# Kernel tuning notes

Measured on AMD Instinct MI355X. Metric: run time of the kernel, lower is better.

Reference implementation:

```python
import jax, jax.numpy as jnp
import numpy as np

B, T_HIST, T_OUT, T_FC = 4096, 168, 48, 49
N_LABELS, F_CTL, F_FC, HID = 64, 16, 8, 32
EPS = 1e-7


def setup_inputs() -> dict:
    key = jax.random.key(0)
    ks = jax.random.split(key, 18)
    rn = lambda k, s, sc=1.0: jax.random.normal(k, s, jnp.float32) * sc
    return {
        "history": rn(ks[0], (B, T_HIST, N_LABELS)),
        "control": rn(ks[1], (B, T_OUT, F_CTL)),
        "forecasts": rn(ks[2], (B, T_FC, F_FC)),
        "h_mean": rn(ks[3], (N_LABELS,), 0.1),
        "h_var": jax.random.uniform(ks[4], (N_LABELS,), jnp.float32, 0.5, 1.5),
        "c_mean": rn(ks[5], (F_CTL,), 0.1),
        "c_var": jax.random.uniform(ks[6], (F_CTL,), jnp.float32, 0.5, 1.5),
        "f_mean": rn(ks[7], (), 0.1),
        "f_var": jax.random.uniform(ks[8], (), jnp.float32, 0.5, 1.5),
        "conv_w": rn(ks[9], (2, F_FC, 4), 0.2),   # kernel_size=2, Conv1D(4)
        "conv_b": rn(ks[10], (4,), 0.01),
        "lstm_k": rn(ks[11], (N_LABELS, 4 * HID), 0.1),
        "lstm_rk": rn(ks[12], (HID, 4 * HID), 0.1),
        "lstm_b": rn(ks[13], (4 * HID,), 0.01),
        "w1": rn(ks[14], (HID + F_CTL + 4, 64), 0.1),
        "b1": rn(ks[15], (64,), 0.01),
        "w2": rn(ks[16], (64, N_LABELS), 0.05),
        "b2": rn(ks[17], (N_LABELS,), 0.01),
    }


def _norm(x, m, v):
    # keras Normalization: (x - mean) / max(sqrt(var), eps)
    return (x - m) / jnp.maximum(jnp.sqrt(v), EPS)


def _lstm(x, h, c, k, rk, b):
    z = x @ k + h @ rk + b                      # [B, 4*HID], gate order i,f,g,o
    i, f, g, o = jnp.split(z, 4, axis=-1)
    c2 = jax.nn.sigmoid(f) * c + jax.nn.sigmoid(i) * jnp.tanh(g)
    h2 = jax.nn.sigmoid(o) * jnp.tanh(c2)
    return h2, c2


def _mlp(x1, x2, x3, w1, b1, w2, b2):
    x = jnp.concatenate([x1, x2, x3], axis=-1)  # [B, 52]
    return jax.nn.relu(x @ w1 + b1) @ w2 + b2


def reference(history, control, forecasts, h_mean, h_var, c_mean, c_var,
              f_mean, f_var, conv_w, conv_b, lstm_k, lstm_rk, lstm_b,
              w1, b1, w2, b2):
    latest = history[:, -1, :]                               # [B, N_LABELS]
    cn = _norm(control, c_mean, c_var)                       # [B, T_OUT, F_CTL]
    fn = _norm(forecasts, f_mean, f_var)                     # scalar norm
    # Conv1D(filters=4, kernel_size=2), valid padding -> [B, T_FC-1, 4]
    fc = fn[:, :-1] @ conv_w[0] + fn[:, 1:] @ conv_w[1] + conv_b

    # encoder LSTM over normalized history
    hn = _norm(history, h_mean, h_var)
    bsz = history.shape[0]
    init = (jnp.zeros((bsz, HID), hn.dtype), jnp.zeros((bsz, HID), hn.dtype))

    def enc_step(carry, x):
        h, c = carry
        return _lstm(x, h, c, lstm_k, lstm_rk, lstm_b), None

    (h, c), _ = jax.lax.scan(enc_step, init, jnp.swapaxes(hn, 0, 1))

    # pre-loop step (its prediction write is overwritten by loop i=0, but it
    # updates `latest` which feeds the loop)
    latest = latest + _mlp(h, cn[:, 0], fc[:, 0], w1, b1, w2, b2)

    t_out = control.shape[1]

    def dec_step(carry, inp):
        latest, h, c = carry
        ctl, fci = inp
        xn = _norm(latest, h_mean, h_var)
        h2, c2 = _lstm(xn, h, c, lstm_k, lstm_rk, lstm_b)
        latest2 = latest + _mlp(h2, ctl, fci, w1, b1, w2, b2)
        return (latest2, h2, c2), latest2

    xs = (jnp.swapaxes(cn, 0, 1), jnp.swapaxes(fc[:, :t_out], 0, 1))
    _, preds = jax.lax.scan(dec_step, (latest, h, c), xs)   # [T_OUT, B, N]
    return jnp.swapaxes(preds, 0, 1)                        # [B, T_OUT, N]
```

## Files before the change

kernel.cpp:

```cpp
#include <hip/hip_runtime.h>

#define EPSV 1e-7f

typedef __bf16 bf16x8 __attribute__((ext_vector_type(8)));
typedef float  f32x4  __attribute__((ext_vector_type(4)));
typedef unsigned int   u32x4 __attribute__((ext_vector_type(4)));
typedef unsigned short u16x8 __attribute__((ext_vector_type(8)));
typedef unsigned short u16x4 __attribute__((ext_vector_type(4)));

__device__ __forceinline__ unsigned short f2bf(float f) {
    unsigned int u = __float_as_uint(f);
    return (unsigned short)((u + 0x7FFFu + ((u >> 16) & 1u)) >> 16);
}
__device__ __forceinline__ float bf2f(unsigned short u) {
    return __uint_as_float(((unsigned int)u) << 16);
}
__device__ __forceinline__ void split2(float f, unsigned short& hi, unsigned short& lo) {
    hi = f2bf(f);
    lo = f2bf(f - bf2f(hi));
}
__device__ __forceinline__ void splitT(float f, unsigned short& hi, unsigned short& lo) {
    unsigned int u  = __float_as_uint(f);
    unsigned int hb = u & 0xFFFF0000u;
    float l = f - __uint_as_float(hb);
    hi = (unsigned short)(u >> 16);
    lo = (unsigned short)(__float_as_uint(l) >> 16);
}
__device__ __forceinline__ float sigf(float x) {
    return __builtin_amdgcn_rcpf(1.0f + __expf(-x));
}
__device__ __forceinline__ float tanhfast(float x) {
    float cx = fminf(fmaxf(x, -15.0f), 15.0f);
    float e = __expf(2.0f * cx);
    return (e - 1.0f) * __builtin_amdgcn_rcpf(e + 1.0f);
}
__device__ __forceinline__ float xor8(float v) {
    return __builtin_bit_cast(float, __builtin_amdgcn_update_dpp(
        0, __builtin_bit_cast(int, v), 0x128, 0xF, 0xF, true));
}

#define MFMA16(A, B, C) __builtin_amdgcn_mfma_f32_16x16x32_bf16(A, B, C, 0, 0, 0)
#define BC8(x) __builtin_bit_cast(bf16x8, x)

#define BARRIER() do {                                        \
    asm volatile("s_waitcnt lgkmcnt(0)" ::: "memory");        \
    __builtin_amdgcn_s_barrier();                             \
    __builtin_amdgcn_sched_barrier(0);                        \
} while (0)

#define HS2 72
#define MS  136
#define XS2 136
#define ZS3 20

__global__ __launch_bounds__(512) void tutina_kernel(
    const float* __restrict__ history, const float* __restrict__ control,
    const float* __restrict__ forecasts,
    const float* __restrict__ h_mean, const float* __restrict__ h_var,
    const float* __restrict__ c_mean, const float* __restrict__ c_var,
    const float* __restrict__ f_mean, const float* __restrict__ f_var,
    const float* __restrict__ conv_w, const float* __restrict__ conv_b,
    const float* __restrict__ lstm_k, const float* __restrict__ lstm_rk,
    const float* __restrict__ lstm_b,
    const float* __restrict__ w1, const float* __restrict__ b1,
    const float* __restrict__ w2, const float* __restrict__ b2,
    float* __restrict__ out)
{
    __shared__ unsigned short hbuf[2][16 * HS2];
    __shared__ float zxb[2][4][2][16 * ZS3];
    __shared__ unsigned short xbuf[16 * XS2];
    __shared__ unsigned short mlps[16 * MS];
    __shared__ unsigned short hids[16 * MS];
    __shared__ unsigned int   fcs[48 * 64];

    const int tid  = threadIdx.x;
    const int lane = tid & 63;
    const int wid  = tid >> 6;
    const int wa   = wid & 3;
    const bool gA  = (wid < 4);
    const int lt   = tid & 255;
    const int l15  = lane & 15;
    const int l4   = lane >> 4;
    const int b0   = blockIdx.x * 16;

    for (int i = tid; i < 16 * HS2; i += 512) hbuf[0][i] = 0;
    for (int i = tid; i < 16 * MS;  i += 512) mlps[i] = 0;

    const int  uu     = l15 & 7;
    const bool lohalf = (l15 < 8);
    const int  u      = wa * 8 + uu;
    const int  jz0    = lohalf ? u      : 32 + u;
    const int  jz1    = lohalf ? 64 + u : 96 + u;
    const int  j1     = wa * 16 + l15;

    auto bfragK = [&](int kbase, int j, float& dacc, bf16x8& H, bf16x8& L) {
        u16x8 h, l;
#pragma unroll
        for (int i = 0; i < 8; i++) {
            int k = kbase + l4 * 8 + i;
            float sv = 1.0f / fmaxf(sqrtf(h_var[k]), EPSV);
            float w  = lstm_k[k * 128 + j] * sv;
            dacc += h_mean[k] * w;
            unsigned short hh, ll; split2(w, hh, ll);
            h[i] = hh; l[i] = ll;
        }
        H = BC8(h); L = BC8(l);
    };
    auto bfragP = [&](const float* W, int ldw, int kbase, int j, bf16x8& H, bf16x8& L) {
        u16x8 h, l;
#pragma unroll
        for (int i = 0; i < 8; i++) {
            int k = kbase + l4 * 8 + i;
            float w = W[k * ldw + j];
            unsigned short hh, ll; split2(w, hh, ll);
            h[i] = hh; l[i] = ll;
        }
        H = BC8(h); L = BC8(l);
    };
    auto bfragW11 = [&](int j, float& dacc, bf16x8& H, bf16x8& L) {
        u16x8 h, l;
#pragma unroll
        for (int i = 0; i < 8; i++) {
            int k = 32 + l4 * 8 + i;
            float w = 0.0f;
            if (k < 52) {
                w = w1[k * 64 + j];
                if (k < 48) {
                    float sv = 1.0f / fmaxf(sqrtf(c_var[k - 32]), EPSV);
                    w *= sv;
                    dacc += c_mean[k - 32] * w;
                }
            }
            unsigned short hh, ll; split2(w, hh, ll);
            h[i] = hh; l[i] = ll;
        }
        H = BC8(h); L = BC8(l);
    };

    bf16x8 fA0h, fA0l, fA1h, fA1l, fB0h, fB0l, fB1h, fB1l;
    float dz0 = 0.f, dz1 = 0.f;
    bfragK(0,  jz0, dz0, fA0h, fA0l);
    bfragK(32, jz0, dz0, fA1h, fA1l);
    bfragK(0,  jz1, dz1, fB0h, fB0l);
    bfragK(32, jz1, dz1, fB1h, fB1l);

    bf16x8 fA2h, fA2l, fB2h, fB2l;
    float bi_ = 0.f, bf_ = 0.f, bg_ = 0.f, bo_ = 0.f;
    f32x4 creg = {0.f, 0.f, 0.f, 0.f};
    const int rc = lt >> 2, cc = (lt & 3) * 4;
    if (gA) {
        bfragP(lstm_rk, 128, 0, jz0, fA2h, fA2l);
        bfragP(lstm_rk, 128, 0, jz1, fB2h, fB2l);
        float z0s = dz0, z1s = dz1;
        z0s += __shfl_xor(z0s, 16, 64); z0s += __shfl_xor(z0s, 32, 64);
        z1s += __shfl_xor(z1s, 16, 64); z1s += __shfl_xor(z1s, 32, 64);
        float pd0 = xor8(z0s), pd1 = xor8(z1s);
        bi_ = lstm_b[u]      - (lohalf ? z0s : pd0);
        bf_ = lstm_b[32 + u] - (lohalf ? pd0 : z0s);
        bg_ = lstm_b[64 + u] - (lohalf ? z1s : pd1);
        bo_ = lstm_b[96 + u] - (lohalf ? pd1 : z1s);
        if (lt < 64)
            creg = *(const f32x4*)(control + ((size_t)(b0 + rc) * 48 + 0) * 16 + cc);
    }

    bf16x8 fW10h, fW10l, fW11h, fW11l, fW20h, fW20l, fW21h, fW21l;
    float b1j = 0.f, b2j = 0.f;
    float lat0 = 0.f, lat1 = 0.f, lat2 = 0.f, lat3 = 0.f;
    if (!gA) {
        bfragP(w1, 64, 0, j1, fW10h, fW10l);
        float d1 = 0.f;
        bfragW11(j1, d1, fW11h, fW11l);
        bfragP(w2, 64, 0,  j1, fW20h, fW20l);
        bfragP(w2, 64, 32, j1, fW21h, fW21l);
        d1 += __shfl_xor(d1, 16, 64); d1 += __shfl_xor(d1, 32, 64);
        b1j = b1[j1] - d1;
        b2j = b2[j1];
        lat0 = history[((size_t)(b0 + l4 * 4 + 0) * 168 + 167) * 64 + j1];
        lat1 = history[((size_t)(b0 + l4 * 4 + 1) * 168 + 167) * 64 + j1];
        lat2 = history[((size_t)(b0 + l4 * 4 + 2) * 168 + 167) * 64 + j1];
        lat3 = history[((size_t)(b0 + l4 * 4 + 3) * 168 + 167) * 64 + j1];
        float fm  = f_mean[0];
        float fsc = 1.0f / fmaxf(sqrtf(f_var[0]), EPSV);
        for (int cell = lt; cell < 48 * 64; cell += 256) {
            int t  = cell >> 6;
            int b  = (cell >> 2) & 15;
            int uc = cell & 3;
            const float* fp = forecasts + ((size_t)(b0 + b) * 49 + t) * 8;
            float acc = conv_b[uc];
#pragma unroll
            for (int k = 0; k < 8; k++) {
                acc += (fp[k]     - fm) * fsc * conv_w[k * 4 + uc];
                acc += (fp[8 + k] - fm) * fsc * conv_w[32 + k * 4 + uc];
            }
            unsigned short hh, ll; split2(acc, hh, ll);
            fcs[cell] = ((unsigned int)hh << 16) | ll;
        }
    }

    const int r0 = l4 * 4 + (lohalf ? 0 : 2);
    const int r1 = r0 + 1;
    float c0 = 0.0f, c1 = 0.0f;

    auto lstm_gates = [&](const f32x4& a, const f32x4& b, unsigned short* hw,
                          bool write_lo, bool write_mlp) {
        float sa0 = lohalf ? a[2] : a[0];
        float sa1 = lohalf ? a[3] : a[1];
        float sb0 = lohalf ? b[2] : b[0];
        float sb1 = lohalf ? b[3] : b[1];
        float ra0 = xor8(sa0);
        float ra1 = xor8(sa1);
        float rb0 = xor8(sb0);
        float rb1 = xor8(sb1);
        float zi0 = (lohalf ? a[0] : ra0) + bi_;
        float zi1 = (lohalf ? a[1] : ra1) + bi_;
        float zf0 = (lohalf ? ra0 : a[2]) + bf_;
        float zf1 = (lohalf ? ra1 : a[3]) + bf_;
        float zg0 = (lohalf ? b[0] : rb0) + bg_;
        float zg1 = (lohalf ? b[1] : rb1) + bg_;
        float zo0 = (lohalf ? rb0 : b[2]) + bo_;
        float zo1 = (lohalf ? rb1 : b[3]) + bo_;
        c0 = sigf(zf0) * c0 + sigf(zi0) * tanhfast(zg0);
        c1 = sigf(zf1) * c1 + sigf(zi1) * tanhfast(zg1);
        float h20 = sigf(zo0) * tanhfast(c0);
        float h21 = sigf(zo1) * tanhfast(c1);
        unsigned short bh, bl;
        splitT(h20, bh, bl);
        hw[r0 * HS2 + u] = bh;
        if (write_lo)  hw[r0 * HS2 + 32 + u] = bl;
        if (write_mlp) { mlps[r0 * MS + u] = bh; mlps[r0 * MS + 64 + u] = bl; }
        splitT(h21, bh, bl);
        hw[r1 * HS2 + u] = bh;
        if (write_lo)  hw[r1 * HS2 + 32 + u] = bl;
        if (write_mlp) { mlps[r1 * MS + u] = bh; mlps[r1 * MS + 64 + u] = bl; }
    };

    auto mk_frags = [&](const f32x4& p0, const f32x4& p1, const f32x4& p2,
                        const f32x4& p3, bf16x8& A0h, bf16x8& A0l,
                        bf16x8& A1h, bf16x8& A1l) {
        u16x8 xh_, xl_;
        unsigned short hh, ll;
#pragma unroll
        for (int i = 0; i < 4; i++) { splitT(p0[i], hh, ll); xh_[i] = hh; xl_[i] = ll; }
#pragma unroll
        for (int i = 0; i < 4; i++) { splitT(p1[i], hh, ll); xh_[4+i] = hh; xl_[4+i] = ll; }
        A0h = BC8(xh_); A0l = BC8(xl_);
#pragma unroll
        for (int i = 0; i < 4; i++) { splitT(p2[i], hh, ll); xh_[i] = hh; xl_[i] = ll; }
#pragma unroll
        for (int i = 0; i < 4; i++) { splitT(p3[i], hh, ll); xh_[4+i] = hh; xl_[4+i] = ll; }
        A1h = BC8(xh_); A1l = BC8(xl_);
    };
    auto zx12 = [&](bf16x8 A0h, bf16x8 A0l, bf16x8 A1h, bf16x8 A1l,
                    f32x4& zn0, f32x4& zn1) {
        f32x4 s0 = {0.f,0.f,0.f,0.f}, s1 = {0.f,0.f,0.f,0.f};
        s0 = MFMA16(A0h, fA0h, s0);  s1 = MFMA16(A0h, fB0h, s1);
        s0 = MFMA16(A1h, fA1h, s0);  s1 = MFMA16(A1h, fB1h, s1);
        s0 = MFMA16(A0l, fA0h, s0);  s1 = MFMA16(A0l, fB0h, s1);
        s0 = MFMA16(A1l, fA1h, s0);  s1 = MFMA16(A1l, fB1h, s1);
        s0 = MFMA16(A0h, fA0l, s0);  s1 = MFMA16(A0h, fB0l, s1);
        s0 = MFMA16(A1h, fA1l, s0);  s1 = MFMA16(A1h, fB1l, s1);
        zn0 = s0; zn1 = s1;
    };

    const float* hp = history + (size_t)(b0 + l15) * (168 * 64);
    const int o1 = l4 * 8, o2 = 32 + l4 * 8;
    const int zoff = l15 * ZS3 + l4 * 4;
    f32x4 vb0, vb1, vb2, vb3;
    if (!gA) {
        f32x4 p0 = *(const f32x4*)(hp + o1), p1 = *(const f32x4*)(hp + o1 + 4);
        f32x4 p2 = *(const f32x4*)(hp + o2), p3 = *(const f32x4*)(hp + o2 + 4);
        bf16x8 A0h, A0l, A1h, A1l;
        mk_frags(p0, p1, p2, p3, A0h, A0l, A1h, A1l);
        f32x4 zn0, zn1;
        zx12(A0h, A0l, A1h, A1l, zn0, zn1);
        *(f32x4*)&zxb[0][wa][0][zoff] = zn0;
        *(f32x4*)&zxb[0][wa][1][zoff] = zn1;
        vb0 = *(const f32x4*)(hp + 64 + o1); vb1 = *(const f32x4*)(hp + 64 + o1 + 4);
        vb2 = *(const f32x4*)(hp + 64 + o2); vb3 = *(const f32x4*)(hp + 64 + o2 + 4);
    }
    if (gA) __builtin_amdgcn_s_setprio(1);
    BARRIER();

    for (int t = 0; t < 168; ++t) {
        const int p = t & 1;
        if (gA) {
            const unsigned short* hr = hbuf[p];
            bf16x8 a2h = BC8(*(const u32x4*)&hr[l15 * HS2 + l4 * 8]);
            f32x4 z0 = *(const f32x4*)&zxb[p][wa][0][zoff];
            f32x4 z1 = *(const f32x4*)&zxb[p][wa][1][zoff];
            z0 = MFMA16(a2h, fA2h, z0);  z1 = MFMA16(a2h, fB2h, z1);
            z0 = MFMA16(a2h, fA2l, z0);  z1 = MFMA16(a2h, fB2l, z1);
            lstm_gates(z0, z1, hbuf[p ^ 1], t == 167, t == 167);
        } else {
            bf16x8 A0h, A0l, A1h, A1l;
            mk_frags(vb0, vb1, vb2, vb3, A0h, A0l, A1h, A1l);
            const float* np = hp + (size_t)((t < 166) ? t + 2 : 167) * 64;
            vb0 = *(const f32x4*)(np + o1); vb1 = *(const f32x4*)(np + o1 + 4);
            vb2 = *(const f32x4*)(np + o2); vb3 = *(const f32x4*)(np + o2 + 4);
            f32x4 zn0, zn1;
            zx12(A0h, A0l, A1h, A1l, zn0, zn1);
            *(f32x4*)&zxb[p ^ 1][wa][0][zoff] = zn0;
            *(f32x4*)&zxb[p ^ 1][wa][1][zoff] = zn1;
        }
        BARRIER();
    }

    auto stage_cn = [&](const f32x4& v) {
        if (lt < 64) {
            u16x4 oh, ol;
#pragma unroll
            for (int q = 0; q < 4; q++) {
                unsigned short hh, ll;
                splitT(v[q], hh, ll);
                oh[q] = hh; ol[q] = ll;
            }
            *(u16x4*)&mlps[rc * MS + 32 + cc]      = oh;
            *(u16x4*)&mlps[rc * MS + 64 + 32 + cc] = ol;
        }
    };
    auto stage_fc = [&](int t) {
        if (lt >= 64 && lt < 128) {
            int q = lt - 64;
            unsigned int v = fcs[t * 64 + q];
            mlps[(q >> 2) * MS + 48 + (q & 3)]      = (unsigned short)(v >> 16);
            mlps[(q >> 2) * MS + 64 + 48 + (q & 3)] = (unsigned short)(v & 0xFFFFu);
        }
    };
    auto mlp1 = [&]() {
        const int mbase = l15 * MS + l4 * 8;
        bf16x8 m0  = BC8(*(const u32x4*)&mlps[mbase]);
        bf16x8 m1  = BC8(*(const u32x4*)&mlps[mbase + 32]);
        bf16x8 m0l = BC8(*(const u32x4*)&mlps[mbase + 64]);
        bf16x8 m1l = BC8(*(const u32x4*)&mlps[mbase + 96]);
        f32x4 ha = {0.f,0.f,0.f,0.f}, hb = {0.f,0.f,0.f,0.f};
        ha = MFMA16(m0,  fW10h, ha);   hb = MFMA16(m1,  fW11h, hb);
        ha = MFMA16(m0l, fW10h, ha);   hb = MFMA16(m1l, fW11h, hb);
        ha = MFMA16(m0,  fW10l, ha);   hb = MFMA16(m1,  fW11l, hb);
        f32x4 hacc = ha + hb;
#pragma unroll
        for (int q = 0; q < 4; q++) {
            float hv = fmaxf(hacc[q] + b1j, 0.0f);
            unsigned short hh, ll;
            splitT(hv, hh, ll);
            hids[(l4 * 4 + q) * MS + j1]      = hh;
            hids[(l4 * 4 + q) * MS + 64 + j1] = ll;
        }
    };
    auto mlp2 = [&]() {
        const int mbase = l15 * MS + l4 * 8;
        bf16x8 h0  = BC8(*(const u32x4*)&hids[mbase]);
        bf16x8 h1  = BC8(*(const u32x4*)&hids[mbase + 32]);
        bf16x8 h0l = BC8(*(const u32x4*)&hids[mbase + 64]);
        bf16x8 h1l = BC8(*(const u32x4*)&hids[mbase + 96]);
        f32x4 oa = {0.f,0.f,0.f,0.f}, ob = {0.f,0.f,0.f,0.f};
        oa = MFMA16(h0,  fW20h, oa);   ob = MFMA16(h1,  fW21h, ob);
        oa = MFMA16(h0l, fW20h, oa);   ob = MFMA16(h1l, fW21h, ob);
        oa = MFMA16(h0,  fW20l, oa);   ob = MFMA16(h1,  fW21l, ob);
        f32x4 oacc = oa + ob;
        lat0 += oacc[0] + b2j;
        lat1 += oacc[1] + b2j;
        lat2 += oacc[2] + b2j;
        lat3 += oacc[3] + b2j;
    };

    if (gA) { stage_cn(creg); stage_fc(0); }
    BARRIER();
    if (!gA) mlp1();
    BARRIER();
    if (!gA) mlp2();
    if (gA && lt < 64)
        creg = *(const f32x4*)(control + ((size_t)(b0 + rc) * 48 + 1) * 16 + cc);

    for (int t = 0; t < 48; ++t) {
        const int p = t & 1;
        if (!gA) {
            unsigned short bh, bl;
            splitT(lat0, bh, bl);
            xbuf[(l4 * 4 + 0) * XS2 + j1] = bh; xbuf[(l4 * 4 + 0) * XS2 + 64 + j1] = bl;
            splitT(lat1, bh, bl);
            xbuf[(l4 * 4 + 1) * XS2 + j1] = bh; xbuf[(l4 * 4 + 1) * XS2 + 64 + j1] = bl;
            splitT(lat2, bh, bl);
            xbuf[(l4 * 4 + 2) * XS2 + j1] = bh; xbuf[(l4 * 4 + 2) * XS2 + 64 + j1] = bl;
            splitT(lat3, bh, bl);
            xbuf[(l4 * 4 + 3) * XS2 + j1] = bh; xbuf[(l4 * 4 + 3) * XS2 + 64 + j1] = bl;
        }
        BARRIER();

        if (gA) {
            const unsigned short* hr = hbuf[p];
            const int xb = l15 * XS2 + l4 * 8;
            bf16x8 a0h = BC8(*(const u32x4*)&xbuf[xb]);
            bf16x8 a1h = BC8(*(const u32x4*)&xbuf[xb + 32]);
            bf16x8 a0l = BC8(*(const u32x4*)&xbuf[xb + 64]);
            bf16x8 a1l = BC8(*(const u32x4*)&xbuf[xb + 96]);
            bf16x8 a2h = BC8(*(const u32x4*)&hr[l15 * HS2 + l4 * 8]);
            bf16x8 a2l = BC8(*(const u32x4*)&hr[l15 * HS2 + 32 + l4 * 8]);
            f32x4 z0a = {0.f,0.f,0.f,0.f}, z0b = {0.f,0.f,0.f,0.f};
            f32x4 z1a = {0.f,0.f,0.f,0.f}, z1b = {0.f,0.f,0.f,0.f};
            z0a = MFMA16(a0h, fA0h, z0a);  z1a = MFMA16(a0h, fB0h, z1a);
            z0b = MFMA16(a1h, fA1h, z0b);  z1b = MFMA16(a1h, fB1h, z1b);
            z0a = MFMA16(a2h, fA2h, z0a);  z1a = MFMA16(a2h, fB2h, z1a);
            z0b = MFMA16(a0l, fA0h, z0b);  z1b = MFMA16(a0l, fB0h, z1b);
            z0a = MFMA16(a1l, fA1h, z0a);  z1a = MFMA16(a1l, fB1h, z1a);
            z0b = MFMA16(a2l, fA2h, z0b);  z1b = MFMA16(a2l, fB2h, z1b);
            z0a = MFMA16(a0h, fA0l, z0a);  z1a = MFMA16(a0h, fB0l, z1a);
            z0b = MFMA16(a1h, fA1l, z0b);  z1b = MFMA16(a1h, fB1l, z1b);
            z0a = MFMA16(a2h, fA2l, z0a);  z1a = MFMA16(a2h, fB2l, z1a);
            f32x4 z0 = z0a + z0b, z1 = z1a + z1b;
            lstm_gates(z0, z1, hbuf[p ^ 1], true, true);
        }
        BARRIER();

        if (!gA) mlp1();
        BARRIER();

        if (!gA) {
            mlp2();
            out[((size_t)(b0 + l4 * 4 + 0) * 48 + t) * 64 + j1] = lat0;
            out[((size_t)(b0 + l4 * 4 + 1) * 48 + t) * 64 + j1] = lat1;
            out[((size_t)(b0 + l4 * 4 + 2) * 48 + t) * 64 + j1] = lat2;
            out[((size_t)(b0 + l4 * 4 + 3) * 48 + t) * 64 + j1] = lat3;
        } else {
            int tn = (t < 47) ? t + 1 : 47;
            stage_cn(creg);
            stage_fc(tn);
            int tn2 = (t < 46) ? t + 2 : 47;
            if (lt < 64)
                creg = *(const f32x4*)(control + ((size_t)(b0 + rc) * 48 + tn2) * 16 + cc);
        }
    }
}

extern "C" void kernel_launch(void* const* d_in, const int* in_sizes, int n_in,
                              void* d_out, int out_size, void* d_ws, size_t ws_size,
                              hipStream_t stream) {
    tutina_kernel<<<dim3(256), dim3(512), 0, stream>>>(
        (const float*)d_in[0],  (const float*)d_in[1],  (const float*)d_in[2],
        (const float*)d_in[3],  (const float*)d_in[4],  (const float*)d_in[5],
        (const float*)d_in[6],  (const float*)d_in[7],  (const float*)d_in[8],
        (const float*)d_in[9],  (const float*)d_in[10], (const float*)d_in[11],
        (const float*)d_in[12], (const float*)d_in[13], (const float*)d_in[14],
        (const float*)d_in[15], (const float*)d_in[16], (const float*)d_in[17],
        (float*)d_out);
}
```

Before: 167.7 us.

## Drop low-part history split, deepen history prefetch, split recurrent MFMA chain

The encoder input projection stops using the low bf16 part of the history activations. It packs the truncated high halves directly, which removes the splitT work and four of the twelve MFMAs per step for the producer waves. The history prefetch is deepened from one step ahead to three steps ahead using rotating register sets, to better hide global-load latency. The recurrent MFMA pair is split into two independent accumulators to shorten the dependency chain. Dropping the activation low part lowers accuracy of the input projection, and the extra registers may pressure occupancy.

```diff
diff --git a/kernel.cpp b/kernel.cpp
--- a/kernel.cpp
+++ b/kernel.cpp
@@ -25,6 +25,9 @@
     float l = f - __uint_as_float(hb);
     hi = (unsigned short)(u >> 16);
     lo = (unsigned short)(__float_as_uint(l) >> 16);
+}
+__device__ __forceinline__ unsigned int packhi2(float a, float b) {
+    return (__float_as_uint(b) & 0xFFFF0000u) | (__float_as_uint(a) >> 16);
 }
 __device__ __forceinline__ float sigf(float x) {
     return __builtin_amdgcn_rcpf(1.0f + __expf(-x));
@@ -82,6 +85,8 @@
     const int l15  = lane & 15;
     const int l4   = lane >> 4;
     const int b0   = blockIdx.x * 16;
+
+    const f32x4 zero4 = {0.f, 0.f, 0.f, 0.f};
 
     for (int i = tid; i < 16 * HS2; i += 512) hbuf[0][i] = 0;
     for (int i = tid; i < 16 * MS;  i += 512) mlps[i] = 0;
@@ -234,29 +239,19 @@
         if (write_mlp) { mlps[r1 * MS + u] = bh; mlps[r1 * MS + 64 + u] = bl; }
     };
 
-    auto mk_frags = [&](const f32x4& p0, const f32x4& p1, const f32x4& p2,
-                        const f32x4& p3, bf16x8& A0h, bf16x8& A0l,
-                        bf16x8& A1h, bf16x8& A1l) {
-        u16x8 xh_, xl_;
-        unsigned short hh, ll;
-#pragma unroll
-        for (int i = 0; i < 4; i++) { splitT(p0[i], hh, ll); xh_[i] = hh; xl_[i] = ll; }
-#pragma unroll
-        for (int i = 0; i < 4; i++) { splitT(p1[i], hh, ll); xh_[4+i] = hh; xl_[4+i] = ll; }
-        A0h = BC8(xh_); A0l = BC8(xl_);
-#pragma unroll
-        for (int i = 0; i < 4; i++) { splitT(p2[i], hh, ll); xh_[i] = hh; xl_[i] = ll; }
-#pragma unroll
-        for (int i = 0; i < 4; i++) { splitT(p3[i], hh, ll); xh_[4+i] = hh; xl_[4+i] = ll; }
-        A1h = BC8(xh_); A1l = BC8(xl_);
-    };
-    auto zx12 = [&](bf16x8 A0h, bf16x8 A0l, bf16x8 A1h, bf16x8 A1l,
-                    f32x4& zn0, f32x4& zn1) {
-        f32x4 s0 = {0.f,0.f,0.f,0.f}, s1 = {0.f,0.f,0.f,0.f};
+    auto mk_frags_hi = [&](const f32x4& p0, const f32x4& p1, const f32x4& p2,
+                           const f32x4& p3, bf16x8& A0h, bf16x8& A1h) {
+        u32x4 w0, w1;
+        w0[0] = packhi2(p0[0], p0[1]); w0[1] = packhi2(p0[2], p0[3]);
+        w0[2] = packhi2(p1[0], p1[1]); w0[3] = packhi2(p1[2], p1[3]);
+        w1[0] = packhi2(p2[0], p2[1]); w1[1] = packhi2(p2[2], p2[3]);
+        w1[2] = packhi2(p3[0], p3[1]); w1[3] = packhi2(p3[2], p3[3]);
+        A0h = BC8(w0); A1h = BC8(w1);
+    };
+    auto zx12_hi = [&](bf16x8 A0h, bf16x8 A1h, f32x4& zn0, f32x4& zn1) {
+        f32x4 s0 = zero4, s1 = zero4;
         s0 = MFMA16(A0h, fA0h, s0);  s1 = MFMA16(A0h, fB0h, s1);
         s0 = MFMA16(A1h, fA1h, s0);  s1 = MFMA16(A1h, fB1h, s1);
-        s0 = MFMA16(A0l, fA0h, s0);  s1 = MFMA16(A0l, fB0h, s1);
-        s0 = MFMA16(A1l, fA1h, s0);  s1 = MFMA16(A1l, fB1h, s1);
         s0 = MFMA16(A0h, fA0l, s0);  s1 = MFMA16(A0h, fB0l, s1);
         s0 = MFMA16(A1h, fA1l, s0);  s1 = MFMA16(A1h, fB1l, s1);
         zn0 = s0; zn1 = s1;
@@ -265,18 +260,24 @@
     const float* hp = history + (size_t)(b0 + l15) * (168 * 64);
     const int o1 = l4 * 8, o2 = 32 + l4 * 8;
     const int zoff = l15 * ZS3 + l4 * 4;
-    f32x4 vb0, vb1, vb2, vb3;
+    f32x4 x1a, x1b, x1c, x1d;
+    f32x4 x2a, x2b, x2c, x2d;
+    f32x4 x3a, x3b, x3c, x3d;
     if (!gA) {
         f32x4 p0 = *(const f32x4*)(hp + o1), p1 = *(const f32x4*)(hp + o1 + 4);
         f32x4 p2 = *(const f32x4*)(hp + o2), p3 = *(const f32x4*)(hp + o2 + 4);
-        bf16x8 A0h, A0l, A1h, A1l;
-        mk_frags(p0, p1, p2, p3, A0h, A0l, A1h, A1l);
+        bf16x8 A0h, A1h;
+        mk_frags_hi(p0, p1, p2, p3, A0h, A1h);
         f32x4 zn0, zn1;
-        zx12(A0h, A0l, A1h, A1l, zn0, zn1);
+        zx12_hi(A0h, A1h, zn0, zn1);
         *(f32x4*)&zxb[0][wa][0][zoff] = zn0;
         *(f32x4*)&zxb[0][wa][1][zoff] = zn1;
-        vb0 = *(const f32x4*)(hp + 64 + o1); vb1 = *(const f32x4*)(hp + 64 + o1 + 4);
-        vb2 = *(const f32x4*)(hp + 64 + o2); vb3 = *(const f32x4*)(hp + 64 + o2 + 4);
+        x1a = *(const f32x4*)(hp + 64 + o1);  x1b = *(const f32x4*)(hp + 64 + o1 + 4);
+        x1c = *(const f32x4*)(hp + 64 + o2);  x1d = *(const f32x4*)(hp + 64 + o2 + 4);
+        x2a = *(const f32x4*)(hp + 128 + o1); x2b = *(const f32x4*)(hp + 128 + o1 + 4);
+        x2c = *(const f32x4*)(hp + 128 + o2); x2d = *(const f32x4*)(hp + 128 + o2 + 4);
+        x3a = *(const f32x4*)(hp + 192 + o1); x3b = *(const f32x4*)(hp + 192 + o1 + 4);
+        x3c = *(const f32x4*)(hp + 192 + o2); x3d = *(const f32x4*)(hp + 192 + o2 + 4);
     }
     if (gA) __builtin_amdgcn_s_setprio(1);
     BARRIER();
@@ -286,19 +287,24 @@
         if (gA) {
             const unsigned short* hr = hbuf[p];
             bf16x8 a2h = BC8(*(const u32x4*)&hr[l15 * HS2 + l4 * 8]);
-            f32x4 z0 = *(const f32x4*)&zxb[p][wa][0][zoff];
-            f32x4 z1 = *(const f32x4*)&zxb[p][wa][1][zoff];
-            z0 = MFMA16(a2h, fA2h, z0);  z1 = MFMA16(a2h, fB2h, z1);
-            z0 = MFMA16(a2h, fA2l, z0);  z1 = MFMA16(a2h, fB2l, z1);
+            f32x4 zx0 = *(const f32x4*)&zxb[p][wa][0][zoff];
+            f32x4 zx1 = *(const f32x4*)&zxb[p][wa][1][zoff];
+            f32x4 z0  = MFMA16(a2h, fA2h, zx0);
+            f32x4 z1  = MFMA16(a2h, fB2h, zx1);
+            f32x4 z0l = MFMA16(a2h, fA2l, zero4);
+            f32x4 z1l = MFMA16(a2h, fB2l, zero4);
+            z0 += z0l; z1 += z1l;
             lstm_gates(z0, z1, hbuf[p ^ 1], t == 167, t == 167);
         } else {
-            bf16x8 A0h, A0l, A1h, A1l;
-            mk_frags(vb0, vb1, vb2, vb3, A0h, A0l, A1h, A1l);
-            const float* np = hp + (size_t)((t < 166) ? t + 2 : 167) * 64;
-            vb0 = *(const f32x4*)(np + o1); vb1 = *(const f32x4*)(np + o1 + 4);
-            vb2 = *(const f32x4*)(np + o2); vb3 = *(const f32x4*)(np + o2 + 4);
+            bf16x8 A0h, A1h;
+            mk_frags_hi(x1a, x1b, x1c, x1d, A0h, A1h);
+            x1a = x2a; x1b = x2b; x1c = x2c; x1d = x2d;
+            x2a = x3a; x2b = x3b; x2c = x3c; x2d = x3d;
+            const float* np = hp + (size_t)((t + 4 < 168) ? t + 4 : 167) * 64;
+            x3a = *(const f32x4*)(np + o1); x3b = *(const f32x4*)(np + o1 + 4);
+            x3c = *(const f32x4*)(np + o2); x3d = *(const f32x4*)(np + o2 + 4);
             f32x4 zn0, zn1;
-            zx12(A0h, A0l, A1h, A1l, zn0, zn1);
+            zx12_hi(A0h, A1h, zn0, zn1);
             *(f32x4*)&zxb[p ^ 1][wa][0][zoff] = zn0;
             *(f32x4*)&zxb[p ^ 1][wa][1][zoff] = zn1;
         }
@@ -332,7 +338,7 @@
         bf16x8 m1  = BC8(*(const u32x4*)&mlps[mbase + 32]);
         bf16x8 m0l = BC8(*(const u32x4*)&mlps[mbase + 64]);
         bf16x8 m1l = BC8(*(const u32x4*)&mlps[mbase + 96]);
-        f32x4 ha = {0.f,0.f,0.f,0.f}, hb = {0.f,0.f,0.f,0.f};
+        f32x4 ha = zero4, hb = zero4;
         ha = MFMA16(m0,  fW10h, ha);   hb = MFMA16(m1,  fW11h, hb);
         ha = MFMA16(m0l, fW10h, ha);   hb = MFMA16(m1l, fW11h, hb);
         ha = MFMA16(m0,  fW10l, ha);   hb = MFMA16(m1,  fW11l, hb);
@@ -352,7 +358,7 @@
         bf16x8 h1  = BC8(*(const u32x4*)&hids[mbase + 32]);
         bf16x8 h0l = BC8(*(const u32x4*)&hids[mbase + 64]);
         bf16x8 h1l = BC8(*(const u32x4*)&hids[mbase + 96]);
-        f32x4 oa = {0.f,0.f,0.f,0.f}, ob = {0.f,0.f,0.f,0.f};
+        f32x4 oa = zero4, ob = zero4;
         oa = MFMA16(h0,  fW20h, oa);   ob = MFMA16(h1,  fW21h, ob);
         oa = MFMA16(h0l, fW20h, oa);   ob = MFMA16(h1l, fW21h, ob);
         oa = MFMA16(h0,  fW20l, oa);   ob = MFMA16(h1,  fW21l, ob);
@@ -395,8 +401,8 @@
             bf16x8 a1l = BC8(*(const u32x4*)&xbuf[xb + 96]);
             bf16x8 a2h = BC8(*(const u32x4*)&hr[l15 * HS2 + l4 * 8]);
             bf16x8 a2l = BC8(*(const u32x4*)&hr[l15 * HS2 + 32 + l4 * 8]);
-            f32x4 z0a = {0.f,0.f,0.f,0.f}, z0b = {0.f,0.f,0.f,0.f};
-            f32x4 z1a = {0.f,0.f,0.f,0.f}, z1b = {0.f,0.f,0.f,0.f};
+            f32x4 z0a = zero4, z0b = zero4;
+            f32x4 z1a = zero4, z1b = zero4;
             z0a = MFMA16(a0h, fA0h, z0a);  z1a = MFMA16(a0h, fB0h, z1a);
             z0b = MFMA16(a1h, fA1h, z0b);  z1b = MFMA16(a1h, fB1h, z1b);
             z0a = MFMA16(a2h, fA2h, z0a);  z1a = MFMA16(a2h, fB2h, z1a);
```

Result: slower. 186.4 us (+11.2%).
